# Kernel tuning notes

Hardware: AMD Instinct MI355X
Metric: run time of the kernel (lower is better)

The kernel has to match this reference:

```python
import jax, jax.numpy as jnp
import numpy as np
from jax.scipy.special import logsumexp

NEG = -1e9  # grad-safe stand-in for -inf in the log-semiring chart
SMOOTH_RATIO = 0.9   # config.structure_smoothing_p


def _inside(lp, lengths):
    """CKY inside algorithm (TreeCRF partition).

    lp: [B, N, N, L] span log-potentials (lp[b, i, j, l] = span (i..j) with label l)
    Returns logZ per batch element: beta(0, len-1).
    Recursion: beta(i,j) = logsumexp_l lp[i,j,l] + logsumexp_{k=i..j-1} beta(i,k)+beta(k+1,j)
    Charts are kept in (start, width) and (end, width) layout so every width
    step is a fully vectorized roll + logsumexp over splits.
    """
    B, N = lp.shape[0], lp.shape[1]
    pot_node = logsumexp(lp, axis=-1)                       # [B, N, N]
    i = jnp.arange(N)
    j = (i[:, None] + i[None, :]) % N
    pot_span = pot_node[:, i[:, None], j]                   # [B, start, width]
    diag = pot_span[:, :, 0]                                # width-0 spans
    init = jnp.full((B, N, N), NEG, dtype=lp.dtype)
    cs = init.at[:, :, 0].set(diag)                         # cs[b,i,u] = beta(i, i+u)
    ce = cs                                                 # ce[b,j,u] = beta(j-u, j)
    u = jnp.arange(N)[None, None, :]
    starts = jnp.arange(N)[None, :]

    def step(carry, xs):
        cs, ce = carry
        w, pot_w = xs
        right = jnp.roll(ce, -w, axis=1)                    # right[b,i] = ce[b, i+w]
        # align so right_al[b,i,u] = ce[b, i+w, w-1-u] = beta(i+u+1, i+w)
        right_al = jnp.roll(right[:, :, ::-1], w - N, axis=2)
        comb = jnp.where(u < w, cs + right_al, NEG)         # splits k = i+u, u in [0,w)
        inner = logsumexp(comb, axis=2)                     # [B, N]
        newv = jnp.where(starts < N - w, inner + pot_w, NEG)
        cs = jax.lax.dynamic_update_slice_in_dim(cs, newv[:, :, None], w, axis=2)
        ce_new = jnp.roll(newv, w, axis=1)[:, :, None]      # reindex start -> end = start+w
        ce = jax.lax.dynamic_update_slice_in_dim(ce, ce_new, w, axis=2)
        return (cs, ce), None

    ws = jnp.arange(1, N)
    pots = jnp.moveaxis(pot_span, 2, 0)[1:]                 # [N-1, B, N]
    (cs, ce), _ = jax.lax.scan(step, (cs, ce), (ws, pots))
    return jnp.take_along_axis(cs[:, 0, :], (lengths - 1)[:, None], axis=1)[:, 0]


def setup_inputs() -> dict:
    key = jax.random.key(0)
    k1, k2, k3, k4 = jax.random.split(key, 4)
    B, N, L = 16, 256, 32
    log_potentials = jax.random.normal(k1, (B, N, N, L), dtype=jnp.float32)
    mask = (jax.random.uniform(k2, (B, N, N, L)) < 0.9).astype(jnp.float32)
    eval_mask = (jax.random.uniform(k3, (B, N, N, L)) < 0.9).astype(jnp.float32)
    lengths = jax.random.randint(k4, (B,), N // 2, N + 1)
    return {"log_potentials": log_potentials, "mask": mask,
            "lengths": lengths, "eval_mask": eval_mask}


def reference(log_potentials, mask, lengths, eval_mask):
    B = log_potentials.shape[0]
    # potential normalization (torch .std() is unbiased, ddof=1)
    flat = log_potentials.reshape(B, -1)
    mean = flat.mean(-1)
    var = ((flat - mean[:, None]) ** 2).sum(-1) / (flat.shape[1] - 1)
    std = jnp.sqrt(var)
    lp = (log_potentials - mean[:, None, None, None]) / std[:, None, None, None]

    z_full = _inside(lp, lengths)
    # CRF entropy: H = logZ - <marginals, theta>, marginals = d logZ / d theta
    marg = jax.grad(lambda p: _inside(p, lengths).sum())(lp)
    entropy = z_full - (marg * lp).sum((1, 2, 3))

    # structure smoothing (structure_smoothing_p = 0.9 < 1.0)
    mask_smooth = eval_mask + (1.0 - eval_mask) * (1.0 - SMOOTH_RATIO)
    z_smooth = _inside(lp + jnp.log(mask_smooth + 1e-10), lengths)
    log_prob_smooth = z_smooth - z_full

    # partially-masked partition
    z_partial = _inside(lp - 1e6 * (1.0 - eval_mask), lengths)
    log_prob = z_partial - z_full
    return (log_prob, log_prob_smooth, entropy)
```

## Files before the change

### kernel.cpp

```cpp
#include <hip/hip_runtime.h>
#include <math.h>

#define B_ 16
#define N_ 256
#define L_ 32
#define NN_ (N_*N_)
#define NNL_ (NN_*L_)
#define ANN_ (B_*NN_)
#define POTS_OFF 4096
#define NEGINF -1.0e30f
#define LOG2E_F 1.4426950408889634f
#define LN2_F   0.6931471805599453f

#if __has_builtin(__builtin_amdgcn_exp2f)
#define EX2(x) __builtin_amdgcn_exp2f(x)
#else
#define EX2(x) exp2f(x)
#endif
#if __has_builtin(__builtin_amdgcn_logf)
#define LG2(x) __builtin_amdgcn_logf(x)
#else
#define LG2(x) log2f(x)
#endif


__global__ void stats_partial(const float* __restrict__ lp, double* __restrict__ part) {
    int blk = blockIdx.x;
    int b = blk >> 5, seg = blk & 31;
    const float4* p4 = (const float4*)(lp + (size_t)b * NNL_ + (size_t)seg * (NNL_ / 32));
    double s = 0.0, ss = 0.0;
    for (int idx = threadIdx.x; idx < (NNL_ / 32 / 4); idx += 256) {
        float4 v = p4[idx];
        s  += (double)v.x + (double)v.y + (double)v.z + (double)v.w;
        ss += (double)v.x * v.x + (double)v.y * v.y + (double)v.z * v.z + (double)v.w * v.w;
    }
    __shared__ double sh0[256], sh1[256];
    sh0[threadIdx.x] = s; sh1[threadIdx.x] = ss;
    __syncthreads();
    for (int off = 128; off > 0; off >>= 1) {
        if (threadIdx.x < off) {
            sh0[threadIdx.x] += sh0[threadIdx.x + off];
            sh1[threadIdx.x] += sh1[threadIdx.x + off];
        }
        __syncthreads();
    }
    if (threadIdx.x == 0) { part[blk * 2] = sh0[0]; part[blk * 2 + 1] = sh1[0]; }
}

__global__ void stats_final(const double* __restrict__ part, float* __restrict__ stats) {
    int b = threadIdx.x;
    if (b >= B_) return;
    double s = 0.0, ss = 0.0;
    for (int k = 0; k < 32; ++k) { s += part[(b * 32 + k) * 2]; ss += part[(b * 32 + k) * 2 + 1]; }
    double n = (double)NNL_;
    double mean = s / n;
    double var = (ss - s * s / n) / (n - 1.0);
    stats[b * 2]     = (float)mean;
    stats[b * 2 + 1] = (float)(1.0 / sqrt(var));
}

__global__ __launch_bounds__(256)
void pots_kernel(const float* __restrict__ lp, const float* __restrict__ evm,
                 const float* __restrict__ stats, float* __restrict__ W) {
    int t = blockIdx.x * 256 + threadIdx.x;
    int b = t >> 16;
    int rem = t & (NN_ - 1);
    int i = rem >> 8;
    int w = rem & (N_ - 1);
    if (i + w >= N_) return;
    int j = i + w;
    const float4* xp = (const float4*)(lp  + ((size_t)(b * NN_ + i * N_ + j) << 5));
    const float4* ep = (const float4*)(evm + ((size_t)(b * NN_ + i * N_ + j) << 5));
    float mean = stats[b * 2], invstd = stats[b * 2 + 1];
    float m1 = NEGINF, s1 = 0.f, n1 = 0.f;
    float m2 = NEGINF, s2 = 0.f;
    float m3 = NEGINF, s3 = 0.f;
#pragma unroll
    for (int c = 0; c < 8; ++c) {
        float4 xv = xp[c];
        float4 em = ep[c];
        float x0 = (xv.x - mean) * invstd, x1 = (xv.y - mean) * invstd;
        float x2 = (xv.z - mean) * invstd, x3 = (xv.w - mean) * invstd;
        {
            float cm = fmaxf(fmaxf(x0, x1), fmaxf(x2, x3));
            float nm = fmaxf(m1, cm);
            float sc = __expf(m1 - nm);
            float e0 = __expf(x0 - nm), e1 = __expf(x1 - nm);
            float e2 = __expf(x2 - nm), e3 = __expf(x3 - nm);
            s1 = s1 * sc + (e0 + e1 + e2 + e3);
            n1 = n1 * sc + (e0 * x0 + e1 * x1 + e2 * x2 + e3 * x3);
            m1 = nm;
        }
        {
            float y0 = x0 + __logf(fmaf(em.x, 0.9f, 0.1f) + 1e-10f);
            float y1 = x1 + __logf(fmaf(em.y, 0.9f, 0.1f) + 1e-10f);
            float y2 = x2 + __logf(fmaf(em.z, 0.9f, 0.1f) + 1e-10f);
            float y3 = x3 + __logf(fmaf(em.w, 0.9f, 0.1f) + 1e-10f);
            float cm = fmaxf(fmaxf(y0, y1), fmaxf(y2, y3));
            float nm = fmaxf(m2, cm);
            float sc = __expf(m2 - nm);
            s2 = s2 * sc + __expf(y0 - nm) + __expf(y1 - nm) + __expf(y2 - nm) + __expf(y3 - nm);
            m2 = nm;
        }
        {
            float z0 = fmaf(em.x, 1e6f, x0 - 1e6f);
            float z1 = fmaf(em.y, 1e6f, x1 - 1e6f);
            float z2 = fmaf(em.z, 1e6f, x2 - 1e6f);
            float z3 = fmaf(em.w, 1e6f, x3 - 1e6f);
            float cm = fmaxf(fmaxf(z0, z1), fmaxf(z2, z3));
            float nm = fmaxf(m3, cm);
            float sc = __expf(m3 - nm);
            s3 = s3 * sc + __expf(z0 - nm) + __expf(z1 - nm) + __expf(z2 - nm) + __expf(z3 - nm);
            m3 = nm;
        }
    }
    int o = b * NN_ + i * N_ + w;
    W[POTS_OFF + 0 * ANN_ + o] = (m1 + __logf(s1)) * LOG2E_F;
    W[POTS_OFF + 1 * ANN_ + o] = n1 / s1;
    W[POTS_OFF + 2 * ANN_ + o] = (m2 + __logf(s2)) * LOG2E_F;
    W[POTS_OFF + 3 * ANN_ + o] = (m3 + __logf(s3)) * LOG2E_F;
}

__device__ __forceinline__ int lds_base(int i) {
    int a = i >> 5, c = i & 31;
    return ((8 * a - ((a * (a - 1)) >> 1)) << 10) + ((c * (8 - a)) << 5);
}
__device__ __forceinline__ int lds_addr(int i, int u) {
    return lds_base(i) + ((((u >> 2) ^ (i & 7)) << 2) | (u & 3));
}

__device__ __forceinline__ float4 ld4u(const float* p) {
    float4 v; __builtin_memcpy(&v, p, 16); return v;
}

template <bool EXPM, int LOGG>
__device__ __forceinline__ void stepw(
    float* __restrict__ SL,
    const float* __restrict__ pot, const float* __restrict__ sbr,
    float* __restrict__ EGe, float* __restrict__ EGh, float* __restrict__ SGh,
    const int w, const int cells, const int tid)
{
    constexpr int G = 1 << LOGG;
    const int group = tid >> LOGG;
    const int l = tid & (G - 1);
    if (group >= cells) return;
    const int i = group;
    const int j = i + w;
    const int ib = lds_base(i);
    const int isw = i & 7;
    const float* egE = EGe + j * N_;
    const float* egH = EGh + j * N_;
    const float* sgH = SGh + i * N_;
    const float pw = pot[i * N_ + w];
    float sb = 0.f;
    if constexpr (EXPM) sb = sbr[i * N_ + w];

    const int F = w >> 2;
    const int r = w & 3;

    float m = NEGINF, s = 0.f, n = 0.f;

    int mu = l;
    bool have = (mu < F);
    float4 Lc, Rc, Hlc, Hrc;
    if (have) {
        Lc = *(const float4*)&SL[ib + ((mu ^ isw) << 2)];
        Rc = ld4u(egE + (w - 4 - (mu << 2)));
        if constexpr (EXPM) {
            Hlc = *(const float4*)(sgH + (mu << 2));
            Hrc = ld4u(egH + (w - 4 - (mu << 2)));
        }
    }
    while (have) {
        const int mun = mu + G;
        const bool hn = (mun < F);
        float4 Ln, Rn, Hln, Hrn;
        if (hn) {
            Ln = *(const float4*)&SL[ib + ((mun ^ isw) << 2)];
            Rn = ld4u(egE + (w - 4 - (mun << 2)));
            if constexpr (EXPM) {
                Hln = *(const float4*)(sgH + (mun << 2));
                Hrn = ld4u(egH + (w - 4 - (mun << 2)));
            }
        }
        {
            float e0 = Lc.x + Rc.w;
            float e1 = Lc.y + Rc.z;
            float e2 = Lc.z + Rc.y;
            float e3 = Lc.w + Rc.x;
            float cm = fmaxf(fmaxf(e0, e1), fmaxf(e2, e3));
            float nm = fmaxf(m, cm);
            float sc = EX2(m - nm);
            float E0 = EX2(e0 - nm), E1 = EX2(e1 - nm);
            float E2 = EX2(e2 - nm), E3 = EX2(e3 - nm);
            s = s * sc + ((E0 + E1) + (E2 + E3));
            if constexpr (EXPM) {
                float h0 = Hlc.x + Hrc.w, h1 = Hlc.y + Hrc.z;
                float h2 = Hlc.z + Hrc.y, h3 = Hlc.w + Hrc.x;
                n = n * sc + ((E0 * h0 + E1 * h1) + (E2 * h2 + E3 * h3));
            }
            m = nm;
        }
        Lc = Ln; Rc = Rn;
        if constexpr (EXPM) { Hlc = Hln; Hrc = Hrn; }
        mu = mun; have = hn;
    }

    if (r && l == (F & (G - 1))) {
        const int u0 = F << 2;
        const float4 Lv = *(const float4*)&SL[ib + ((F ^ isw) << 2)];
        const float4 Rv = ld4u(egE + (w - 4 - u0));
        float e0 = Lv.x + Rv.w;
        float e1 = Lv.y + Rv.z;
        float e2 = Lv.z + Rv.y;
        float e3 = NEGINF;
        if (r < 2) e1 = NEGINF;
        if (r < 3) e2 = NEGINF;
        float cm = fmaxf(fmaxf(e0, e1), e2);
        float nm = fmaxf(m, cm);
        float sc = EX2(m - nm);
        float E0 = EX2(e0 - nm), E1 = EX2(e1 - nm);
        float E2 = EX2(e2 - nm), E3 = EX2(e3 - nm);
        s = s * sc + ((E0 + E1) + (E2 + E3));
        if constexpr (EXPM) {
            const float4 Hl = *(const float4*)(sgH + u0);
            const float4 Hr = ld4u(egH + (w - 4 - u0));
            float h0 = Hl.x + Hr.w, h1 = Hl.y + Hr.z, h2 = Hl.z + Hr.y;
            if (r < 2) h1 = 0.f;
            if (r < 3) h2 = 0.f;
            n = n * sc + ((E0 * h0 + E1 * h1) + E2 * h2);
        }
        m = nm;
    }

#pragma unroll
    for (int k = 1; k < G; k <<= 1) {
        float mo = __shfl_xor(m, k);
        float so = __shfl_xor(s, k);
        float no = 0.f;
        if constexpr (EXPM) no = __shfl_xor(n, k);
        float nm = fmaxf(m, mo);
        float a  = EX2(m - nm), bb = EX2(mo - nm);
        s = s * a + so * bb;
        if constexpr (EXPM) n = n * a + no * bb;
        m = nm;
    }
    if (l == 0) {
        float v = pw + m + LG2(s);
        SL[lds_addr(i, w)] = v;
        EGe[j * N_ + w] = v;
        if constexpr (EXPM) {
            float hv = sb + n / s;
            SGh[i * N_ + w] = hv;
            EGh[j * N_ + w] = hv;
        }
    }
}

template <bool EXPM>
__device__ __forceinline__ void cky_loop(
    float* __restrict__ SL,
    const float* __restrict__ pot, const float* __restrict__ sbr,
    float* __restrict__ EGe, float* __restrict__ EGh, float* __restrict__ SGh,
    const int len, const int tid)
{
    for (int i = tid; i < len; i += 1024) {
        float v = pot[i * N_];
        SL[lds_addr(i, 0)] = v;
        EGe[i * N_] = v;
        if constexpr (EXPM) { float h0 = sbr[i * N_]; SGh[i * N_] = h0; EGh[i * N_] = h0; }
    }
    __syncthreads();
    for (int w = 1; w < len; ++w) {
        const int cells = len - w;
        if (cells > 128)      stepw<EXPM, 2>(SL, pot, sbr, EGe, EGh, SGh, w, cells, tid);
        else if (cells > 64)  stepw<EXPM, 3>(SL, pot, sbr, EGe, EGh, SGh, w, cells, tid);
        else if (cells > 32)  stepw<EXPM, 4>(SL, pot, sbr, EGe, EGh, SGh, w, cells, tid);
        else if (cells > 16)  stepw<EXPM, 5>(SL, pot, sbr, EGe, EGh, SGh, w, cells, tid);
        else                  stepw<EXPM, 6>(SL, pot, sbr, EGe, EGh, SGh, w, cells, tid);
        __syncthreads();
    }
}

__global__ __launch_bounds__(1024, 1)
void cky_all(float* __restrict__ W, const int* __restrict__ lengths) {
    __shared__ float SL[36864];
    const int bx = blockIdx.x;
    const int p = bx >> 4, b = bx & 15;
    const int tid = threadIdx.x;
    int len = lengths[b];
    if (len < 1) len = 1;
    if (len > N_) len = N_;
    float* zres = W + POTS_OFF + 9 * ANN_;

    if (p == 0) {
        const float* pot = W + POTS_OFF + 0 * ANN_ + b * NN_;
        const float* sbr = W + POTS_OFF + 1 * ANN_ + b * NN_;
        float* EGe = W + POTS_OFF + 4 * ANN_ + b * NN_;
        float* EGh = W + POTS_OFF + 5 * ANN_ + b * NN_;
        float* SGh = W + POTS_OFF + 6 * ANN_ + b * NN_;
        cky_loop<true>(SL, pot, sbr, EGe, EGh, SGh, len, tid);
        if (tid == 0) {
            zres[b]      = SL[lds_addr(0, len - 1)];
            zres[48 + b] = SGh[len - 1];
        }
    } else {
        const float* pot = W + POTS_OFF + (p == 1 ? 2 : 3) * ANN_ + b * NN_;
        float* EGe = W + POTS_OFF + (p == 1 ? 7 : 8) * ANN_ + b * NN_;
        cky_loop<false>(SL, pot, nullptr, EGe, nullptr, nullptr, len, tid);
        if (tid == 0) zres[p * 16 + b] = SL[lds_addr(0, len - 1)];
    }
}

__global__ void combine_kernel(const float* __restrict__ W, float* __restrict__ out) {
    int b = threadIdx.x;
    if (b >= B_) return;
    const float* zres = W + POTS_OFF + 9 * ANN_;
    float zf = zres[b], zs = zres[16 + b], zp = zres[32 + b], hr = zres[48 + b];
    out[b]          = (zp - zf) * LN2_F;
    out[16 + b]     = (zs - zf) * LN2_F;
    out[32 + b]     = zf * LN2_F - hr;
}

extern "C" void kernel_launch(void* const* d_in, const int* in_sizes, int n_in,
                              void* d_out, int out_size, void* d_ws, size_t ws_size,
                              hipStream_t stream) {
    const float* lp      = (const float*)d_in[0];
    const int*   lengths = (const int*)d_in[2];
    const float* evm     = (const float*)d_in[3];
    float*  W    = (float*)d_ws;
    double* part = (double*)d_ws;
    float*  stats = W + 2048;
    float*  out  = (float*)d_out;

    stats_partial<<<B_ * 32, 256, 0, stream>>>(lp, part);
    stats_final<<<1, 64, 0, stream>>>(part, stats);
    pots_kernel<<<(B_ * NN_) / 256, 256, 0, stream>>>(lp, evm, stats, W);
    cky_all<<<3 * B_, 1024, 0, stream>>>(W, lengths);
    combine_kernel<<<1, 64, 0, stream>>>(W, out);
}
```

Baseline: 965.6 us.

## Interleave end-indexed value and entropy charts and unroll split loop by two

```diff
diff --git a/kernel.cpp b/kernel.cpp
--- a/kernel.cpp
+++ b/kernel.cpp
@@ -137,7 +137,8 @@
 __device__ __forceinline__ void stepw(
     float* __restrict__ SL,
     const float* __restrict__ pot, const float* __restrict__ sbr,
-    float* __restrict__ EGe, float* __restrict__ EGh, float* __restrict__ SGh,
+    float* __restrict__ EG,
+    float* __restrict__ SGh,
     const int w, const int cells, const int tid)
 {
     constexpr int G = 1 << LOGG;
@@ -148,8 +149,7 @@
     const int j = i + w;
     const int ib = lds_base(i);
     const int isw = i & 7;
-    const float* egE = EGe + j * N_;
-    const float* egH = EGh + j * N_;
+    const float* egE = EG + (EXPM ? ((j * N_) << 1) : (j * N_));
     const float* sgH = SGh + i * N_;
     const float pw = pot[i * N_ + w];
     float sb = 0.f;
@@ -161,75 +161,88 @@
     float m = NEGINF, s = 0.f, n = 0.f;
 
     int mu = l;
-    bool have = (mu < F);
-    float4 Lc, Rc, Hlc, Hrc;
-    if (have) {
-        Lc = *(const float4*)&SL[ib + ((mu ^ isw) << 2)];
-        Rc = ld4u(egE + (w - 4 - (mu << 2)));
-        if constexpr (EXPM) {
-            Hlc = *(const float4*)(sgH + (mu << 2));
-            Hrc = ld4u(egH + (w - 4 - (mu << 2)));
-        }
-    }
-    while (have) {
-        const int mun = mu + G;
-        const bool hn = (mun < F);
-        float4 Ln, Rn, Hln, Hrn;
-        if (hn) {
-            Ln = *(const float4*)&SL[ib + ((mun ^ isw) << 2)];
-            Rn = ld4u(egE + (w - 4 - (mun << 2)));
-            if constexpr (EXPM) {
-                Hln = *(const float4*)(sgH + (mun << 2));
-                Hrn = ld4u(egH + (w - 4 - (mun << 2)));
-            }
-        }
-        {
-            float e0 = Lc.x + Rc.w;
-            float e1 = Lc.y + Rc.z;
-            float e2 = Lc.z + Rc.y;
-            float e3 = Lc.w + Rc.x;
-            float cm = fmaxf(fmaxf(e0, e1), fmaxf(e2, e3));
-            float nm = fmaxf(m, cm);
-            float sc = EX2(m - nm);
-            float E0 = EX2(e0 - nm), E1 = EX2(e1 - nm);
-            float E2 = EX2(e2 - nm), E3 = EX2(e3 - nm);
-            s = s * sc + ((E0 + E1) + (E2 + E3));
-            if constexpr (EXPM) {
-                float h0 = Hlc.x + Hrc.w, h1 = Hlc.y + Hrc.z;
-                float h2 = Hlc.z + Hrc.y, h3 = Hlc.w + Hrc.x;
-                n = n * sc + ((E0 * h0 + E1 * h1) + (E2 * h2 + E3 * h3));
-            }
-            m = nm;
-        }
-        Lc = Ln; Rc = Rn;
-        if constexpr (EXPM) { Hlc = Hln; Hrc = Hrn; }
-        mu = mun; have = hn;
-    }
-
+    for (; mu + G < F; mu += 2 * G) {
+        const int ua = mu << 2, ub = (mu + G) << 2;
+        const float4 La = *(const float4*)&SL[ib + ((mu ^ isw) << 2)];
+        const float4 Lb = *(const float4*)&SL[ib + (((mu + G) ^ isw) << 2)];
+        float ea0, ea1, ea2, ea3, eb0, eb1, eb2, eb3;
+        float ha0, ha1, ha2, ha3, hb0, hb1, hb2, hb3;
+        if constexpr (EXPM) {
+            const float4 Pa0 = ld4u(egE + ((w - 4 - ua) << 1));
+            const float4 Pa1 = ld4u(egE + ((w - 4 - ua) << 1) + 4);
+            const float4 Pb0 = ld4u(egE + ((w - 4 - ub) << 1));
+            const float4 Pb1 = ld4u(egE + ((w - 4 - ub) << 1) + 4);
+            const float4 Ha = *(const float4*)(sgH + ua);
+            const float4 Hb = *(const float4*)(sgH + ub);
+            ea0 = La.x + Pa1.z; ea1 = La.y + Pa1.x; ea2 = La.z + Pa0.z; ea3 = La.w + Pa0.x;
+            eb0 = Lb.x + Pb1.z; eb1 = Lb.y + Pb1.x; eb2 = Lb.z + Pb0.z; eb3 = Lb.w + Pb0.x;
+            ha0 = Ha.x + Pa1.w; ha1 = Ha.y + Pa1.y; ha2 = Ha.z + Pa0.w; ha3 = Ha.w + Pa0.y;
+            hb0 = Hb.x + Pb1.w; hb1 = Hb.y + Pb1.y; hb2 = Hb.z + Pb0.w; hb3 = Hb.w + Pb0.y;
+        } else {
+            const float4 Ra = ld4u(egE + (w - 4 - ua));
+            const float4 Rb = ld4u(egE + (w - 4 - ub));
+            ea0 = La.x + Ra.w; ea1 = La.y + Ra.z; ea2 = La.z + Ra.y; ea3 = La.w + Ra.x;
+            eb0 = Lb.x + Rb.w; eb1 = Lb.y + Rb.z; eb2 = Lb.z + Rb.y; eb3 = Lb.w + Rb.x;
+        }
+        float cma = fmaxf(fmaxf(ea0, ea1), fmaxf(ea2, ea3));
+        float cmb = fmaxf(fmaxf(eb0, eb1), fmaxf(eb2, eb3));
+        float nm = fmaxf(m, fmaxf(cma, cmb));
+        float sc = EX2(m - nm);
+        float A0 = EX2(ea0 - nm), A1 = EX2(ea1 - nm), A2 = EX2(ea2 - nm), A3 = EX2(ea3 - nm);
+        float B0 = EX2(eb0 - nm), B1 = EX2(eb1 - nm), B2 = EX2(eb2 - nm), B3 = EX2(eb3 - nm);
+        s = s * sc + (((A0 + A1) + (A2 + A3)) + ((B0 + B1) + (B2 + B3)));
+        if constexpr (EXPM) {
+            n = n * sc + (((A0 * ha0 + A1 * ha1) + (A2 * ha2 + A3 * ha3))
+                        + ((B0 * hb0 + B1 * hb1) + (B2 * hb2 + B3 * hb3)));
+        }
+        m = nm;
+    }
+    if (mu < F) {
+        const int u0 = mu << 2;
+        const float4 Lv = *(const float4*)&SL[ib + ((mu ^ isw) << 2)];
+        float e0, e1, e2, e3, h0, h1, h2, h3;
+        if constexpr (EXPM) {
+            const float4 P0 = ld4u(egE + ((w - 4 - u0) << 1));
+            const float4 P1 = ld4u(egE + ((w - 4 - u0) << 1) + 4);
+            const float4 Hl = *(const float4*)(sgH + u0);
+            e0 = Lv.x + P1.z; e1 = Lv.y + P1.x; e2 = Lv.z + P0.z; e3 = Lv.w + P0.x;
+            h0 = Hl.x + P1.w; h1 = Hl.y + P1.y; h2 = Hl.z + P0.w; h3 = Hl.w + P0.y;
+        } else {
+            const float4 Rv = ld4u(egE + (w - 4 - u0));
+            e0 = Lv.x + Rv.w; e1 = Lv.y + Rv.z; e2 = Lv.z + Rv.y; e3 = Lv.w + Rv.x;
+        }
+        float cm = fmaxf(fmaxf(e0, e1), fmaxf(e2, e3));
+        float nm = fmaxf(m, cm);
+        float sc = EX2(m - nm);
+        float E0 = EX2(e0 - nm), E1 = EX2(e1 - nm), E2 = EX2(e2 - nm), E3 = EX2(e3 - nm);
+        s = s * sc + ((E0 + E1) + (E2 + E3));
+        if constexpr (EXPM)
+            n = n * sc + ((E0 * h0 + E1 * h1) + (E2 * h2 + E3 * h3));
+        m = nm;
+    }
     if (r && l == (F & (G - 1))) {
         const int u0 = F << 2;
         const float4 Lv = *(const float4*)&SL[ib + ((F ^ isw) << 2)];
-        const float4 Rv = ld4u(egE + (w - 4 - u0));
-        float e0 = Lv.x + Rv.w;
-        float e1 = Lv.y + Rv.z;
-        float e2 = Lv.z + Rv.y;
-        float e3 = NEGINF;
-        if (r < 2) e1 = NEGINF;
-        if (r < 3) e2 = NEGINF;
+        float e0, e1, e2, h0 = 0.f, h1 = 0.f, h2 = 0.f;
+        if constexpr (EXPM) {
+            const float4 P0 = ld4u(egE + ((w - 4 - u0) << 1));
+            const float4 P1 = ld4u(egE + ((w - 4 - u0) << 1) + 4);
+            const float4 Hl = *(const float4*)(sgH + u0);
+            e0 = Lv.x + P1.z; e1 = Lv.y + P1.x; e2 = Lv.z + P0.z;
+            h0 = Hl.x + P1.w; h1 = Hl.y + P1.y; h2 = Hl.z + P0.w;
+        } else {
+            const float4 Rv = ld4u(egE + (w - 4 - u0));
+            e0 = Lv.x + Rv.w; e1 = Lv.y + Rv.z; e2 = Lv.z + Rv.y;
+        }
+        if (r < 2) { e1 = NEGINF; h1 = 0.f; }
+        if (r < 3) { e2 = NEGINF; h2 = 0.f; }
         float cm = fmaxf(fmaxf(e0, e1), e2);
         float nm = fmaxf(m, cm);
         float sc = EX2(m - nm);
-        float E0 = EX2(e0 - nm), E1 = EX2(e1 - nm);
-        float E2 = EX2(e2 - nm), E3 = EX2(e3 - nm);
-        s = s * sc + ((E0 + E1) + (E2 + E3));
-        if constexpr (EXPM) {
-            const float4 Hl = *(const float4*)(sgH + u0);
-            const float4 Hr = ld4u(egH + (w - 4 - u0));
-            float h0 = Hl.x + Hr.w, h1 = Hl.y + Hr.z, h2 = Hl.z + Hr.y;
-            if (r < 2) h1 = 0.f;
-            if (r < 3) h2 = 0.f;
+        float E0 = EX2(e0 - nm), E1 = EX2(e1 - nm), E2 = EX2(e2 - nm);
+        s = s * sc + ((E0 + E1) + E2);
+        if constexpr (EXPM)
             n = n * sc + ((E0 * h0 + E1 * h1) + E2 * h2);
-        }
         m = nm;
     }
 
@@ -248,11 +261,12 @@
     if (l == 0) {
         float v = pw + m + LG2(s);
         SL[lds_addr(i, w)] = v;
-        EGe[j * N_ + w] = v;
         if constexpr (EXPM) {
             float hv = sb + n / s;
+            ((float2*)EG)[j * N_ + w] = make_float2(v, hv);
             SGh[i * N_ + w] = hv;
-            EGh[j * N_ + w] = hv;
+        } else {
+            EG[j * N_ + w] = v;
         }
     }
 }
@@ -261,23 +275,28 @@
 __device__ __forceinline__ void cky_loop(
     float* __restrict__ SL,
     const float* __restrict__ pot, const float* __restrict__ sbr,
-    float* __restrict__ EGe, float* __restrict__ EGh, float* __restrict__ SGh,
+    float* __restrict__ EG, float* __restrict__ SGh,
     const int len, const int tid)
 {
     for (int i = tid; i < len; i += 1024) {
         float v = pot[i * N_];
         SL[lds_addr(i, 0)] = v;
-        EGe[i * N_] = v;
-        if constexpr (EXPM) { float h0 = sbr[i * N_]; SGh[i * N_] = h0; EGh[i * N_] = h0; }
+        if constexpr (EXPM) {
+            float h0 = sbr[i * N_];
+            ((float2*)EG)[i * N_] = make_float2(v, h0);
+            SGh[i * N_] = h0;
+        } else {
+            EG[i * N_] = v;
+        }
     }
     __syncthreads();
     for (int w = 1; w < len; ++w) {
         const int cells = len - w;
-        if (cells > 128)      stepw<EXPM, 2>(SL, pot, sbr, EGe, EGh, SGh, w, cells, tid);
-        else if (cells > 64)  stepw<EXPM, 3>(SL, pot, sbr, EGe, EGh, SGh, w, cells, tid);
-        else if (cells > 32)  stepw<EXPM, 4>(SL, pot, sbr, EGe, EGh, SGh, w, cells, tid);
-        else if (cells > 16)  stepw<EXPM, 5>(SL, pot, sbr, EGe, EGh, SGh, w, cells, tid);
-        else                  stepw<EXPM, 6>(SL, pot, sbr, EGe, EGh, SGh, w, cells, tid);
+        if (cells > 128)      stepw<EXPM, 2>(SL, pot, sbr, EG, SGh, w, cells, tid);
+        else if (cells > 64)  stepw<EXPM, 3>(SL, pot, sbr, EG, SGh, w, cells, tid);
+        else if (cells > 32)  stepw<EXPM, 4>(SL, pot, sbr, EG, SGh, w, cells, tid);
+        else if (cells > 16)  stepw<EXPM, 5>(SL, pot, sbr, EG, SGh, w, cells, tid);
+        else                  stepw<EXPM, 6>(SL, pot, sbr, EG, SGh, w, cells, tid);
         __syncthreads();
     }
 }
@@ -296,18 +315,17 @@
     if (p == 0) {
         const float* pot = W + POTS_OFF + 0 * ANN_ + b * NN_;
         const float* sbr = W + POTS_OFF + 1 * ANN_ + b * NN_;
-        float* EGe = W + POTS_OFF + 4 * ANN_ + b * NN_;
-        float* EGh = W + POTS_OFF + 5 * ANN_ + b * NN_;
+        float* EG2 = W + POTS_OFF + 4 * ANN_ + b * (NN_ * 2);
         float* SGh = W + POTS_OFF + 6 * ANN_ + b * NN_;
-        cky_loop<true>(SL, pot, sbr, EGe, EGh, SGh, len, tid);
+        cky_loop<true>(SL, pot, sbr, EG2, SGh, len, tid);
         if (tid == 0) {
             zres[b]      = SL[lds_addr(0, len - 1)];
             zres[48 + b] = SGh[len - 1];
         }
     } else {
         const float* pot = W + POTS_OFF + (p == 1 ? 2 : 3) * ANN_ + b * NN_;
-        float* EGe = W + POTS_OFF + (p == 1 ? 7 : 8) * ANN_ + b * NN_;
-        cky_loop<false>(SL, pot, nullptr, EGe, nullptr, nullptr, len, tid);
+        float* EG = W + POTS_OFF + (p == 1 ? 7 : 8) * ANN_ + b * NN_;
+        cky_loop<false>(SL, pot, nullptr, EG, nullptr, len, tid);
         if (tid == 0) zres[p * 16 + b] = SL[lds_addr(0, len - 1)];
     }
 }
```

New measurement: 910.7 us. 5.7% less time.
